# Performance work log

Hardware: AMD Instinct MI355X
Metric: run time of the kernel (lower is better)

Reference implementation:

```python
import jax, jax.numpy as jnp
import numpy as np
import math

B, S, H_DIM, N_HEADS, ATTN_DIM = 64, 64, 768, 12, 64

def setup_inputs() -> dict:
    key = jax.random.key(0)
    k1, k2, k3, k4 = jax.random.split(key, 4)
    x = jax.random.normal(k1, (B, S, H_DIM), dtype=jnp.float32)
    # per-head fused QKV projection weight: [N, 3*D, h_dim] (nn.Linear stores [out,in])
    W_proj = jax.random.normal(k2, (N_HEADS, 3 * ATTN_DIM, H_DIM), dtype=jnp.float32) * (1.0 / math.sqrt(H_DIM))
    in_f = N_HEADS * S * ATTN_DIM
    out_f = S * ATTN_DIM
    W_lin = jax.random.normal(k3, (out_f, in_f), dtype=jnp.float32) * (1.0 / math.sqrt(in_f))
    b_lin = jax.random.normal(k4, (out_f,), dtype=jnp.float32) * 0.01
    return {"x": x, "W_proj": W_proj, "W_lin": W_lin, "b_lin": b_lin}

def reference(x, W_proj, W_lin, b_lin):
    Bsz, Sq, _ = x.shape
    D = ATTN_DIM
    # fused per-head QKV: [B, N, S, 3D]
    qkv = jnp.einsum('bsd,nfd->bnsf', x, W_proj)
    q, k, v = qkv[..., :D], qkv[..., D:2 * D], qkv[..., 2 * D:]
    # raw scaled scores [B, N, S, S]
    scores = jnp.einsum('bnqd,bnkd->bnqk', q, k) / jnp.sqrt(jnp.asarray(D, x.dtype))
    causal = jnp.triu(jnp.ones((Sq, Sq), dtype=bool), k=1)
    masked_scores = jnp.where(causal, -jnp.inf, scores)
    attn = jax.nn.softmax(masked_scores, axis=-1)  # dropout=0.0 (eval) -> identity
    ctx = jnp.einsum('bnqk,bnkd->bnqd', attn, v)   # [B, N, S, D]
    z_flat = ctx.reshape(Bsz, -1)                  # [B, N*S*D]
    y = z_flat @ W_lin.T + b_lin                   # [B, S*D]
    y = y.reshape(Bsz, 1, Sq, D)
    return (y, masked_scores)
```

## Files before the change

### kernel.cpp

```cpp
#include <hip/hip_runtime.h>
#include <math.h>


#define NEG_BIG (-1.0e30f)

typedef __attribute__((ext_vector_type(8))) short bf16x8;
typedef __attribute__((ext_vector_type(4))) float f32x4;
typedef const __attribute__((address_space(1))) void gvoid_t;
typedef __attribute__((address_space(3))) void svoid_t;

static __device__ __forceinline__ unsigned short f2bf(float x) {
    unsigned u = __builtin_bit_cast(unsigned, x);
    return (unsigned short)((u + 0x7FFFu + ((u >> 16) & 1u)) >> 16);
}
static __device__ __forceinline__ ushort4 f2bf4(float4 v) {
    ushort4 r; r.x = f2bf(v.x); r.y = f2bf(v.y); r.z = f2bf(v.z); r.w = f2bf(v.w); return r;
}

__global__ __launch_bounds__(256, 4) void k_qkv(const float* __restrict__ X,
                                                const float* __restrict__ Wp,
                                                unsigned short* __restrict__ qkvb) {
    __shared__ unsigned short Ah[128][72];
    __shared__ unsigned short Bh[128][72];
    const int t  = threadIdx.x;
    const int wv = t >> 6, ln = t & 63;
    const int lr = ln & 15;
    const int kq = (ln >> 4) * 8;
    const int rbase = (ln >> 4) * 4;
    const int m0 = (blockIdx.x / 18) * 128;
    const int j0 = (blockIdx.x % 18) * 128;
    const f32x4 zero4 = {0.f, 0.f, 0.f, 0.f};

    f32x4 acc[2][8];
#pragma unroll
    for (int rt = 0; rt < 2; ++rt)
#pragma unroll
        for (int ct = 0; ct < 8; ++ct) acc[rt][ct] = zero4;

    for (int k0 = 0; k0 < 768; k0 += 64) {
#pragma unroll
        for (int i = 0; i < 8; ++i) {
            const int q   = t + 256 * i;
            const int row = q >> 4;
            const int kc  = (q & 15) * 4;
            float4 xa = *reinterpret_cast<const float4*>(&X[(size_t)(m0 + row) * 768 + k0 + kc]);
            *reinterpret_cast<ushort4*>(&Ah[row][kc]) = f2bf4(xa);
            float4 wb = *reinterpret_cast<const float4*>(&Wp[(size_t)(j0 + row) * 768 + k0 + kc]);
            *reinterpret_cast<ushort4*>(&Bh[row][kc]) = f2bf4(wb);
        }
        __syncthreads();
#pragma unroll
        for (int ks = 0; ks < 2; ++ks) {
            const int kb = ks * 32 + kq;
            bf16x8 a0 = *reinterpret_cast<const bf16x8*>(&Ah[wv * 32 + lr][kb]);
            bf16x8 a1 = *reinterpret_cast<const bf16x8*>(&Ah[wv * 32 + 16 + lr][kb]);
#pragma unroll
            for (int ct = 0; ct < 8; ++ct) {
                bf16x8 bh = *reinterpret_cast<const bf16x8*>(&Bh[ct * 16 + lr][kb]);
                acc[0][ct] = __builtin_amdgcn_mfma_f32_16x16x32_bf16(a0, bh, acc[0][ct], 0, 0, 0);
                acc[1][ct] = __builtin_amdgcn_mfma_f32_16x16x32_bf16(a1, bh, acc[1][ct], 0, 0, 0);
            }
        }
        __syncthreads();
    }
#pragma unroll
    for (int rt = 0; rt < 2; ++rt)
#pragma unroll
        for (int ct = 0; ct < 8; ++ct)
#pragma unroll
            for (int r = 0; r < 4; ++r) {
                const int m = m0 + wv * 32 + rt * 16 + rbase + r;
                const int j = j0 + ct * 16 + lr;
                const int b = m >> 6, s = m & 63;
                const int n = j / 192, f = j % 192;
                qkvb[(((size_t)b * 12 + n) * 64 + s) * 192 + f] = f2bf(acc[rt][ct][r]);
            }
}

__global__ __launch_bounds__(256, 4) void k_attn(const unsigned short* __restrict__ qkvb,
                                                 float* __restrict__ msk,
                                                 unsigned short* __restrict__ Zh) {
    __shared__ unsigned short Qh[64][72];
    __shared__ unsigned short Kh[64][72];
    __shared__ unsigned short Vth[64][72];
    __shared__ unsigned short Ph[64][72];
    const int t  = threadIdx.x;
    const int wv = t >> 6, ln = t & 63;
    const int lr = ln & 15;
    const int kq = (ln >> 4) * 8;
    const int rbase = (ln >> 4) * 4;
    const int bn = blockIdx.x;
    const int bb = bn / 12, nn = bn % 12;
    const unsigned short* base = qkvb + (size_t)bn * 12288;
    const f32x4 zero4 = {0.f, 0.f, 0.f, 0.f};

#pragma unroll
    for (int i = 0; i < 6; ++i) {
        const int q   = t + 256 * i;
        const int row = q / 24;
        const int c8  = (q % 24) * 8;
        const int sec = c8 >> 6;
        const int d0  = c8 & 63;
        bf16x8 v = *reinterpret_cast<const bf16x8*>(&base[(size_t)row * 192 + c8]);
        if (sec == 0) {
            *reinterpret_cast<bf16x8*>(&Qh[row][d0]) = v;
        } else if (sec == 1) {
            *reinterpret_cast<bf16x8*>(&Kh[row][d0]) = v;
        } else {
#pragma unroll
            for (int jj = 0; jj < 8; ++jj) Vth[d0 + jj][row] = (unsigned short)v[jj];
        }
    }
    __syncthreads();

    f32x4 acc[4];
#pragma unroll
    for (int ct = 0; ct < 4; ++ct) acc[ct] = zero4;
#pragma unroll
    for (int ks = 0; ks < 2; ++ks) {
        const int kb = ks * 32 + kq;
        bf16x8 qh = *reinterpret_cast<const bf16x8*>(&Qh[wv * 16 + lr][kb]);
#pragma unroll
        for (int ct = 0; ct < 4; ++ct) {
            bf16x8 kh = *reinterpret_cast<const bf16x8*>(&Kh[ct * 16 + lr][kb]);
            acc[ct] = __builtin_amdgcn_mfma_f32_16x16x32_bf16(qh, kh, acc[ct], 0, 0, 0);
        }
    }

    float s_[4][4];
#pragma unroll
    for (int ct = 0; ct < 4; ++ct)
#pragma unroll
        for (int r = 0; r < 4; ++r) {
            const int row = wv * 16 + rbase + r;
            const int col = ct * 16 + lr;
            float s = (col > row) ? NEG_BIG : acc[ct][r] * 0.125f;
            s_[ct][r] = s;
            msk[(size_t)bn * 4096 + (size_t)row * 64 + col] = s;
        }
    float m[4], sum[4], p[4][4];
#pragma unroll
    for (int r = 0; r < 4; ++r)
        m[r] = fmaxf(fmaxf(s_[0][r], s_[1][r]), fmaxf(s_[2][r], s_[3][r]));
#pragma unroll
    for (int off = 1; off <= 8; off <<= 1)
#pragma unroll
        for (int r = 0; r < 4; ++r) m[r] = fmaxf(m[r], __shfl_xor(m[r], off));
#pragma unroll
    for (int r = 0; r < 4; ++r) sum[r] = 0.f;
#pragma unroll
    for (int ct = 0; ct < 4; ++ct)
#pragma unroll
        for (int r = 0; r < 4; ++r) { p[ct][r] = expf(s_[ct][r] - m[r]); sum[r] += p[ct][r]; }
#pragma unroll
    for (int off = 1; off <= 8; off <<= 1)
#pragma unroll
        for (int r = 0; r < 4; ++r) sum[r] += __shfl_xor(sum[r], off);
#pragma unroll
    for (int ct = 0; ct < 4; ++ct)
#pragma unroll
        for (int r = 0; r < 4; ++r)
            Ph[wv * 16 + rbase + r][ct * 16 + lr] = f2bf(p[ct][r] * (1.f / sum[r]));

    f32x4 o_[4];
#pragma unroll
    for (int ct = 0; ct < 4; ++ct) o_[ct] = zero4;
#pragma unroll
    for (int ks = 0; ks < 2; ++ks) {
        const int kb = ks * 32 + kq;
        bf16x8 ph = *reinterpret_cast<const bf16x8*>(&Ph[wv * 16 + lr][kb]);
#pragma unroll
        for (int ct = 0; ct < 4; ++ct) {
            bf16x8 vh = *reinterpret_cast<const bf16x8*>(&Vth[ct * 16 + lr][kb]);
            o_[ct] = __builtin_amdgcn_mfma_f32_16x16x32_bf16(ph, vh, o_[ct], 0, 0, 0);
        }
    }
    const int rt_z = bb >> 4;
#pragma unroll
    for (int ct = 0; ct < 4; ++ct)
#pragma unroll
        for (int r = 0; r < 4; ++r) {
            const int srow = wv * 16 + rbase + r;
            const int d    = ct * 16 + lr;
            const int k    = nn * 4096 + srow * 64 + d;
            const int lz   = (((k >> 3) & 3) << 4) + (bb & 15);
            const size_t zi = (((size_t)rt_z * 1536 + (k >> 5)) * 64 + lz) * 8 + (k & 7);
            Zh[zi] = f2bf(o_[ct][r]);
        }
}

__global__ __launch_bounds__(256, 2) void k_lin(const unsigned short* __restrict__ Zh,
                                                const float* __restrict__ Wl,
                                                float* __restrict__ part) {
    __shared__ __align__(16) unsigned short Zlds[2][16][64][8];
    __shared__ __align__(16) unsigned short Wbuf[4][2][16][136];
    const int t  = threadIdx.x;
    const int wv = t >> 6, ln = t & 63;
    const int lr = ln & 15;
    const int rbase = (ln >> 4) * 4;
    const int kg   = blockIdx.x & 7;
    const int unit = blockIdx.x >> 3;
    const int o0   = unit * 64;
    const f32x4 zero4 = {0.f, 0.f, 0.f, 0.f};

    const int rlo = (ln >= 32) ? 1 : 0;
    const float* wbase = Wl + (size_t)(o0 + wv * 16) * 49152 + kg * 6144 + (ln & 31) * 4;
    char* wrow = (char*)&Wbuf[wv][0][0][0];

    f32x4 acc[4];
#pragma unroll
    for (int rt = 0; rt < 4; ++rt) acc[rt] = zero4;

    float4 wregA[8], wregB[8];
#define WLOAD(REG, sub_)                                                            \
    {                                                                               \
        _Pragma("unroll")                                                           \
        for (int i = 0; i < 8; ++i)                                                 \
            REG[i] = *reinterpret_cast<const float4*>(                              \
                wbase + (size_t)(2 * i + rlo) * 49152 + (sub_) * 128);              \
    }
#define WWRITE(buf_, REG)                                                           \
    {                                                                               \
        _Pragma("unroll")                                                           \
        for (int i = 0; i < 8; ++i) {                                               \
            unsigned u0 = (unsigned)f2bf(REG[i].x) | ((unsigned)f2bf(REG[i].y) << 16); \
            unsigned u1 = (unsigned)f2bf(REG[i].z) | ((unsigned)f2bf(REG[i].w) << 16); \
            uint2 pk; pk.x = u0; pk.y = u1;                                         \
            *reinterpret_cast<uint2*>(wrow + ((buf_) * 16 + 2 * i + rlo) * 272 + (ln & 31) * 8) = pk; \
        }                                                                           \
    }
#define ZSTAGE(buf_, sub_)                                                          \
    {                                                                               \
        const int kf0 = kg * 192 + (sub_) * 4;                                      \
        _Pragma("unroll")                                                           \
        for (int q = 0; q < 4; ++q) {                                               \
            const unsigned short* src = Zh +                                        \
                ((size_t)(wv * 1536 + kf0 + q) * 64 + ln) * 8;                      \
            __builtin_amdgcn_global_load_lds((gvoid_t*)src,                         \
                (svoid_t*)&Zlds[buf_][wv * 4 + q][0][0], 16, 0, 0);                 \
        }                                                                           \
    }
#define COMPUTE(buf_)                                                               \
    {                                                                               \
        _Pragma("unroll")                                                           \
        for (int kfo = 0; kfo < 4; ++kfo) {                                         \
            bf16x8 wf = *reinterpret_cast<const bf16x8*>(                           \
                wrow + ((buf_) * 16 + lr) * 272 + kfo * 64 + (ln >> 4) * 16);       \
            _Pragma("unroll")                                                       \
            for (int rt = 0; rt < 4; ++rt) {                                        \
                bf16x8 z = *reinterpret_cast<const bf16x8*>(&Zlds[buf_][rt * 4 + kfo][ln][0]); \
                acc[rt] = __builtin_amdgcn_mfma_f32_16x16x32_bf16(z, wf, acc[rt], 0, 0, 0); \
            }                                                                       \
        }                                                                           \
    }

    ZSTAGE(0, 0)
    WLOAD(wregA, 0)
    asm volatile("s_waitcnt vmcnt(0)" ::: "memory");
    WWRITE(0, wregA)
    WLOAD(wregB, 1)
    __syncthreads();

    for (int sp = 0; sp < 23; ++sp) {
        const int s0 = sp * 2;
        ZSTAGE(1, s0 + 1)
        WLOAD(wregA, s0 + 2)
        COMPUTE(0)
        asm volatile("s_waitcnt vmcnt(8)" ::: "memory");
        WWRITE(1, wregB)
        __syncthreads();
        ZSTAGE(0, s0 + 2)
        WLOAD(wregB, s0 + 3)
        COMPUTE(1)
        asm volatile("s_waitcnt vmcnt(8)" ::: "memory");
        WWRITE(0, wregA)
        __syncthreads();
    }
    ZSTAGE(1, 47)
    COMPUTE(0)
    asm volatile("s_waitcnt vmcnt(0)" ::: "memory");
    WWRITE(1, wregB)
    __syncthreads();
    COMPUTE(1)
#undef WLOAD
#undef WWRITE
#undef ZSTAGE
#undef COMPUTE

    const int ocol = o0 + wv * 16 + lr;
#pragma unroll
    for (int rt = 0; rt < 4; ++rt)
#pragma unroll
        for (int r = 0; r < 4; ++r)
            part[((size_t)kg * 64 + rt * 16 + rbase + r) * 4096 + ocol] = acc[rt][r];
}

__global__ __launch_bounds__(256) void k_reduce(const float* __restrict__ part,
                                                const float* __restrict__ bias,
                                                float* __restrict__ y) {
    const int idx = blockIdx.x * 256 + threadIdx.x;
    const int o = idx & 4095;
    const int b = idx >> 12;
    float s = bias[o];
#pragma unroll
    for (int kg = 0; kg < 8; ++kg)
        s += part[((size_t)kg * 64 + b) * 4096 + o];
    y[idx] = s;
}

extern "C" void kernel_launch(void* const* d_in, const int* in_sizes, int n_in,
                              void* d_out, int out_size, void* d_ws, size_t ws_size,
                              hipStream_t stream) {
    const float* x  = (const float*)d_in[0];
    const float* Wp = (const float*)d_in[1];
    const float* Wl = (const float*)d_in[2];
    const float* bl = (const float*)d_in[3];
    float* out = (float*)d_out;

    unsigned short* qkvb = (unsigned short*)d_ws;
    unsigned short* Zh   = (unsigned short*)((char*)d_ws + 18874368);
    float*          part = (float*)((char*)d_ws + 25165824);
    float* y    = out;
    float* msk  = out + 262144;

    hipLaunchKernelGGL(k_qkv,    dim3(576),  dim3(256), 0, stream, x, Wp, qkvb);
    hipLaunchKernelGGL(k_attn,   dim3(768),  dim3(256), 0, stream, qkvb, msk, Zh);
    hipLaunchKernelGGL(k_lin,    dim3(512),  dim3(256), 0, stream, Zh, Wl, part);
    hipLaunchKernelGGL(k_reduce, dim3(1024), dim3(256), 0, stream, part, bl, y);
}
```

Baseline: 278.9 us.

## Restructure k_lin W staging into single 256-wide LDS buffer with new pipeline

```diff
diff --git a/kernel.cpp b/kernel.cpp
--- a/kernel.cpp
+++ b/kernel.cpp
@@ -193,7 +193,7 @@
                                                 const float* __restrict__ Wl,
                                                 float* __restrict__ part) {
     __shared__ __align__(16) unsigned short Zlds[2][16][64][8];
-    __shared__ __align__(16) unsigned short Wbuf[4][2][16][136];
+    __shared__ __align__(16) unsigned short Wbuf[4][16][264];
     const int t  = threadIdx.x;
     const int wv = t >> 6, ln = t & 63;
     const int lr = ln & 15;
@@ -203,30 +203,29 @@
     const int o0   = unit * 64;
     const f32x4 zero4 = {0.f, 0.f, 0.f, 0.f};
 
-    const int rlo = (ln >= 32) ? 1 : 0;
-    const float* wbase = Wl + (size_t)(o0 + wv * 16) * 49152 + kg * 6144 + (ln & 31) * 4;
-    char* wrow = (char*)&Wbuf[wv][0][0][0];
+    const float* wbase = Wl + (size_t)(o0 + wv * 16) * 49152 + kg * 6144 + ln * 4;
+    char* wrow = (char*)&Wbuf[wv][0][0];
 
     f32x4 acc[4];
 #pragma unroll
     for (int rt = 0; rt < 4; ++rt) acc[rt] = zero4;
 
-    float4 wregA[8], wregB[8];
-#define WLOAD(REG, sub_)                                                            \
+    float4 wregA[16], wregB[16];
+#define WLOAD(REG, R_)                                                              \
     {                                                                               \
         _Pragma("unroll")                                                           \
-        for (int i = 0; i < 8; ++i)                                                 \
+        for (int i = 0; i < 16; ++i)                                                \
             REG[i] = *reinterpret_cast<const float4*>(                              \
-                wbase + (size_t)(2 * i + rlo) * 49152 + (sub_) * 128);              \
-    }
-#define WWRITE(buf_, REG)                                                           \
+                wbase + (size_t)i * 49152 + (R_) * 256);                            \
+    }
+#define WWRITE(REG)                                                                 \
     {                                                                               \
         _Pragma("unroll")                                                           \
-        for (int i = 0; i < 8; ++i) {                                               \
+        for (int i = 0; i < 16; ++i) {                                              \
             unsigned u0 = (unsigned)f2bf(REG[i].x) | ((unsigned)f2bf(REG[i].y) << 16); \
             unsigned u1 = (unsigned)f2bf(REG[i].z) | ((unsigned)f2bf(REG[i].w) << 16); \
             uint2 pk; pk.x = u0; pk.y = u1;                                         \
-            *reinterpret_cast<uint2*>(wrow + ((buf_) * 16 + 2 * i + rlo) * 272 + (ln & 31) * 8) = pk; \
+            *reinterpret_cast<uint2*>(wrow + i * 528 + ln * 8) = pk;                \
         }                                                                           \
     }
 #define ZSTAGE(buf_, sub_)                                                          \
@@ -240,48 +239,58 @@
                 (svoid_t*)&Zlds[buf_][wv * 4 + q][0][0], 16, 0, 0);                 \
         }                                                                           \
     }
-#define COMPUTE(buf_)                                                               \
+#define COMPUTE(zbuf_, h_)                                                          \
     {                                                                               \
         _Pragma("unroll")                                                           \
         for (int kfo = 0; kfo < 4; ++kfo) {                                         \
             bf16x8 wf = *reinterpret_cast<const bf16x8*>(                           \
-                wrow + ((buf_) * 16 + lr) * 272 + kfo * 64 + (ln >> 4) * 16);       \
+                wrow + lr * 528 + (h_) * 256 + kfo * 64 + (ln >> 4) * 16);          \
             _Pragma("unroll")                                                       \
             for (int rt = 0; rt < 4; ++rt) {                                        \
-                bf16x8 z = *reinterpret_cast<const bf16x8*>(&Zlds[buf_][rt * 4 + kfo][ln][0]); \
+                bf16x8 z = *reinterpret_cast<const bf16x8*>(&Zlds[zbuf_][rt * 4 + kfo][ln][0]); \
                 acc[rt] = __builtin_amdgcn_mfma_f32_16x16x32_bf16(z, wf, acc[rt], 0, 0, 0); \
             }                                                                       \
         }                                                                           \
     }
 
+    WLOAD(wregA, 0)
     ZSTAGE(0, 0)
-    WLOAD(wregA, 0)
     asm volatile("s_waitcnt vmcnt(0)" ::: "memory");
-    WWRITE(0, wregA)
+    WWRITE(wregA)
     WLOAD(wregB, 1)
     __syncthreads();
 
-    for (int sp = 0; sp < 23; ++sp) {
-        const int s0 = sp * 2;
-        ZSTAGE(1, s0 + 1)
-        WLOAD(wregA, s0 + 2)
-        COMPUTE(0)
-        asm volatile("s_waitcnt vmcnt(8)" ::: "memory");
-        WWRITE(1, wregB)
+    for (int R = 0; R < 22; ++R) {
+        const int e = 2 * R;
+        ZSTAGE(1, e + 1)
+        COMPUTE(0, 0)
+        asm volatile("s_waitcnt vmcnt(0)" ::: "memory");
         __syncthreads();
-        ZSTAGE(0, s0 + 2)
-        WLOAD(wregB, s0 + 3)
-        COMPUTE(1)
-        asm volatile("s_waitcnt vmcnt(8)" ::: "memory");
-        WWRITE(0, wregA)
+        ZSTAGE(0, e + 2)
+        if (R & 1) { WLOAD(wregB, R + 2) } else { WLOAD(wregA, R + 2) }
+        COMPUTE(1, 1)
+        asm volatile("s_waitcnt lgkmcnt(0)" ::: "memory");
+        __builtin_amdgcn_sched_barrier(0);
+        if (R & 1) { WWRITE(wregA) } else { WWRITE(wregB) }
+        asm volatile("s_waitcnt vmcnt(16)" ::: "memory");
         __syncthreads();
     }
+    ZSTAGE(1, 45)
+    COMPUTE(0, 0)
+    asm volatile("s_waitcnt vmcnt(0)" ::: "memory");
+    __syncthreads();
+    ZSTAGE(0, 46)
+    COMPUTE(1, 1)
+    asm volatile("s_waitcnt lgkmcnt(0)" ::: "memory");
+    __builtin_amdgcn_sched_barrier(0);
+    WWRITE(wregB)
+    asm volatile("s_waitcnt vmcnt(0)" ::: "memory");
+    __syncthreads();
     ZSTAGE(1, 47)
-    COMPUTE(0)
+    COMPUTE(0, 0)
     asm volatile("s_waitcnt vmcnt(0)" ::: "memory");
-    WWRITE(1, wregB)
-    __syncthreads();
-    COMPUTE(1)
+    __syncthreads();
+    COMPUTE(1, 1)
 #undef WLOAD
 #undef WWRITE
 #undef ZSTAGE
```

Result: slower. 393.0 us (+40.9%).
